# Optimization experiments

Hardware: AMD Instinct MI355X
Metric: run time of the kernel (lower is better)

Reference implementation:

```python
import jax, jax.numpy as jnp
import numpy as np

N = 50000      # nodes
E = 600000     # edges (avg degree 12)
D = 128        # input_dim == hidden_dim (required: same Linear reused across pool layers)
OUT = 64       # output_dim
NUM_POOL = 2   # num_pool_layers


def setup_inputs() -> dict:
    key = jax.random.key(0)
    ks = jax.random.split(key, 8)
    s = 1.0 / np.sqrt(D)  # fan-in style scaling keeps repeated scatter-adds stable
    x = jax.random.normal(ks[0], (N, D), dtype=jnp.float32)
    edge_index = jax.random.randint(ks[1], (2, E), 0, N, dtype=jnp.int64)
    W1 = jax.random.normal(ks[2], (D, D), dtype=jnp.float32) * s
    b1 = jnp.zeros((D,), dtype=jnp.float32)
    W2 = jax.random.normal(ks[3], (D, D), dtype=jnp.float32) * s
    b2 = jnp.zeros((D,), dtype=jnp.float32)
    Wout = jax.random.normal(ks[4], (D, OUT), dtype=jnp.float32) * s
    bout = jnp.zeros((OUT,), dtype=jnp.float32)
    return {"x": x, "edge_index": edge_index, "W1": W1, "b1": b1,
            "W2": W2, "b2": b2, "Wout": Wout, "bout": bout}


def _gauss_seidel_pool(x, W, b, src, dst, num_layers):
    # PyG MessagePassing(aggr='add'): out[i] = sum_{edges (j->i)} lin(x[j]).
    # Nodes with no incoming edges become zero (propagate replaces x entirely).
    for _ in range(num_layers):
        m = x @ W + b                      # [N, out] linear once per node (== lin(x_j) per edge)
        x = jax.ops.segment_sum(m[src], dst, num_segments=N)  # gather + scatter-add
    return x


def reference(x, edge_index, W1, b1, W2, b2, Wout, bout):
    src = edge_index[0]  # x_j source
    dst = edge_index[1]  # aggregation target i
    h = _gauss_seidel_pool(x, W1, b1, src, dst, NUM_POOL)
    h = jax.nn.relu(h)                     # dropout = identity (eval mode)
    h = _gauss_seidel_pool(h, W2, b2, src, dst, NUM_POOL)
    h = jax.nn.relu(h)
    return h @ Wout + bout                 # [N, OUT]
```

## Files before the change

kernel.cpp:

```cpp
#include <hip/hip_runtime.h>


static inline int ceil_div(int a, int b) { return (a + b - 1) / b; }

typedef __attribute__((ext_vector_type(8))) short bf16x8;
typedef __attribute__((ext_vector_type(4))) float f32x4;

__device__ inline unsigned short f2bf(float f) {
    unsigned u = __float_as_uint(f);
    return (unsigned short)((u + 0x7fffu + ((u >> 16) & 1u)) >> 16);
}


__device__ void wprep_dev(const float* __restrict__ W, unsigned short* __restrict__ hi,
                          int total, int C, int g0, int G) {
    for (int t = g0; t < total; t += G) {
        int j = t & 7;
        int lane = (t >> 3) & 63;
        int f = t >> 9;
        int c = f & 3, ct = f >> 2;
        int k = c * 32 + (lane >> 4) * 8 + j;
        int col = ct * 16 + (lane & 15);
        hi[t] = f2bf(W[(size_t)k * C + col]);
    }
}

__global__ __launch_bounds__(256) void prep_kernel(const float* __restrict__ x,
                                                   const float* __restrict__ W1,
                                                   const float* __restrict__ W2,
                                                   const float* __restrict__ Wout,
                                                   unsigned short* __restrict__ xb,
                                                   unsigned short* __restrict__ W1hi,
                                                   unsigned short* __restrict__ W2hi,
                                                   unsigned short* __restrict__ Wohi,
                                                   int* __restrict__ cursor,
                                                   unsigned* __restrict__ stat,
                                                   int N, int nChunks) {
    int g0 = blockIdx.x * 256 + threadIdx.x;
    int G = gridDim.x * 256;
    for (int i = g0; i < N; i += G) cursor[i] = 0;
    for (int i = g0; i < nChunks; i += G) stat[i] = 0;

    int nq = N * 32;
    for (int i = g0; i < nq; i += G) {
        float4 v = ((const float4*)x)[i];
        ushort4 o;
        o.x = f2bf(v.x); o.y = f2bf(v.y); o.z = f2bf(v.z); o.w = f2bf(v.w);
        ((ushort4*)xb)[i] = o;
    }

    wprep_dev(W1, W1hi, 128 * 128, 128, g0, G);
    wprep_dev(W2, W2hi, 128 * 128, 128, g0, G);
    wprep_dev(Wout, Wohi, 128 * 64, 64, g0, G);
}


__global__ __launch_bounds__(256) void hist_kernel(const int* __restrict__ dst,
                                                   int* __restrict__ deg, int E) {
    int e = blockIdx.x * 256 + threadIdx.x;
    if (e < E) atomicAdd(&deg[dst[e]], 1);
}

__global__ __launch_bounds__(256) void scan_fuse_kernel(const int* __restrict__ deg,
                                                        int* __restrict__ rp,
                                                        int* __restrict__ cursor,
                                                        unsigned* __restrict__ stat,
                                                        int N) {
    __shared__ int s[256];
    int c = blockIdx.x, tid = threadIdx.x;
    int i = c * 256 + tid;
    int v = (i < N) ? deg[i] : 0;
    s[tid] = v;
    __syncthreads();
    for (int off = 1; off < 256; off <<= 1) {
        int t = (tid >= off) ? s[tid - off] : 0;
        __syncthreads();
        s[tid] += t;
        __syncthreads();
    }
    int loc = s[tid] - v;
    int tot = s[255];
    __syncthreads();
    if (tid == 0) atomicExch(&stat[c], (unsigned)tot | 0x80000000u);

    unsigned mine = 0;
    if (tid < c) {
        unsigned u;
        do { u = atomicAdd(&stat[tid], 0u); } while (!(u & 0x80000000u));
        mine = u & 0x7fffffffu;
    }
    s[tid] = (int)mine;
    __syncthreads();
    for (int off = 128; off >= 1; off >>= 1) {
        if (tid < off) s[tid] += s[tid + off];
        __syncthreads();
    }
    int prefix = s[0];
    if (i <= N) {
        int val = loc + prefix;
        rp[i] = val;
        if (i < N) cursor[i] = val;
    }
}

__global__ __launch_bounds__(256) void fill_kernel(const int* __restrict__ src,
                                                   const int* __restrict__ dst,
                                                   int* __restrict__ cursor,
                                                   unsigned short* __restrict__ es, int E) {
    int e = blockIdx.x * 256 + threadIdx.x;
    if (e < E) {
        int p = atomicAdd(&cursor[dst[e]], 1);
        es[p] = (unsigned short)src[e];
    }
}


__device__ inline void acc_row8(float* a, uint4 v) {
    a[0] += __uint_as_float(v.x << 16);
    a[1] += __uint_as_float(v.x & 0xffff0000u);
    a[2] += __uint_as_float(v.y << 16);
    a[3] += __uint_as_float(v.y & 0xffff0000u);
    a[4] += __uint_as_float(v.z << 16);
    a[5] += __uint_as_float(v.z & 0xffff0000u);
    a[6] += __uint_as_float(v.w << 16);
    a[7] += __uint_as_float(v.w & 0xffff0000u);
}

template <bool RELU, bool OUTCHAIN>
__global__ __launch_bounds__(256) void fused_kernel(const unsigned short* __restrict__ M,
                                                    const int* __restrict__ rp,
                                                    const unsigned short* __restrict__ es,
                                                    const uint4* __restrict__ Whi,
                                                    const float* __restrict__ bvec,
                                                    const uint4* __restrict__ Wof,
                                                    const float* __restrict__ bout,
                                                    void* __restrict__ Yv, int n) {
    constexpr int SR = 136;
    __shared__ unsigned short Hl[64 * SR];
    __shared__ int rpl[65];
    __shared__ unsigned char perm[64];

    int tid = threadIdx.x;
    int r0 = blockIdx.x * 64;

    if (tid < 65) {
        int gi = r0 + tid;
        if (gi > n) gi = n;
        rpl[tid] = rp[gi];
    }
    __syncthreads();

    if (tid < 64) {
        int di = rpl[tid + 1] - rpl[tid];
        int rank = 0;
        for (int j = 0; j < 64; ++j) {
            int dj = rpl[j + 1] - rpl[j];
            rank += (dj > di) || (dj == di && j < tid);
        }
        perm[rank] = (unsigned char)tid;
    }
    __syncthreads();

    {
        int g = tid >> 4, ln = tid & 15;
#pragma unroll 1
        for (int q = 0; q < 4; ++q) {
            int nl = perm[q * 16 + g];
            int beg = rpl[nl], end = rpl[nl + 1];
            float acc[8] = {};
            int e = beg;
            for (; e + 8 <= end; e += 8) {
                int s0 = es[e],     s1 = es[e + 1], s2 = es[e + 2], s3 = es[e + 3];
                int s4 = es[e + 4], s5 = es[e + 5], s6 = es[e + 6], s7 = es[e + 7];
                uint4 v0 = ((const uint4*)(M + (size_t)s0 * 128))[ln];
                uint4 v1 = ((const uint4*)(M + (size_t)s1 * 128))[ln];
                uint4 v2 = ((const uint4*)(M + (size_t)s2 * 128))[ln];
                uint4 v3 = ((const uint4*)(M + (size_t)s3 * 128))[ln];
                uint4 v4 = ((const uint4*)(M + (size_t)s4 * 128))[ln];
                uint4 v5 = ((const uint4*)(M + (size_t)s5 * 128))[ln];
                uint4 v6 = ((const uint4*)(M + (size_t)s6 * 128))[ln];
                uint4 v7 = ((const uint4*)(M + (size_t)s7 * 128))[ln];
                acc_row8(acc, v0); acc_row8(acc, v1);
                acc_row8(acc, v2); acc_row8(acc, v3);
                acc_row8(acc, v4); acc_row8(acc, v5);
                acc_row8(acc, v6); acc_row8(acc, v7);
            }
            for (; e + 4 <= end; e += 4) {
                int s0 = es[e], s1 = es[e + 1], s2 = es[e + 2], s3 = es[e + 3];
                uint4 v0 = ((const uint4*)(M + (size_t)s0 * 128))[ln];
                uint4 v1 = ((const uint4*)(M + (size_t)s1 * 128))[ln];
                uint4 v2 = ((const uint4*)(M + (size_t)s2 * 128))[ln];
                uint4 v3 = ((const uint4*)(M + (size_t)s3 * 128))[ln];
                acc_row8(acc, v0); acc_row8(acc, v1);
                acc_row8(acc, v2); acc_row8(acc, v3);
            }
            for (; e < end; ++e) {
                uint4 v = ((const uint4*)(M + (size_t)es[e] * 128))[ln];
                acc_row8(acc, v);
            }
            uint4 o;
            o.x = (unsigned)f2bf(acc[0]) | ((unsigned)f2bf(acc[1]) << 16);
            o.y = (unsigned)f2bf(acc[2]) | ((unsigned)f2bf(acc[3]) << 16);
            o.z = (unsigned)f2bf(acc[4]) | ((unsigned)f2bf(acc[5]) << 16);
            o.w = (unsigned)f2bf(acc[6]) | ((unsigned)f2bf(acc[7]) << 16);
            *(uint4*)(&Hl[nl * SR + ln * 8]) = o;
        }
    }
    __syncthreads();

    int wave = tid >> 6, lane = tid & 63;
    int lm = lane & 15, lq = lane >> 4;

    f32x4 acc[4][2];
#pragma unroll
    for (int rt = 0; rt < 4; ++rt)
#pragma unroll
        for (int t = 0; t < 2; ++t)
            acc[rt][t] = (f32x4){0.f, 0.f, 0.f, 0.f};

#pragma unroll
    for (int c = 0; c < 4; ++c) {
        bf16x8 afr[4];
#pragma unroll
        for (int rt = 0; rt < 4; ++rt)
            afr[rt] = *(const bf16x8*)(&Hl[(rt * 16 + lm) * SR + c * 32 + lq * 8]);
#pragma unroll
        for (int t = 0; t < 2; ++t) {
            int ct = wave * 2 + t;
            uint4 uh = Whi[(ct * 4 + c) * 64 + lane];
            bf16x8 wh = *(const bf16x8*)&uh;
#pragma unroll
            for (int rt = 0; rt < 4; ++rt)
                acc[rt][t] = __builtin_amdgcn_mfma_f32_16x16x32_bf16(afr[rt], wh, acc[rt][t], 0, 0, 0);
        }
    }

    if (!OUTCHAIN) {
#pragma unroll
        for (int t = 0; t < 2; ++t) {
            int col = (wave * 2 + t) * 16 + lm;
            float bv = bvec[col];
#pragma unroll
            for (int rt = 0; rt < 4; ++rt) {
#pragma unroll
                for (int r = 0; r < 4; ++r) {
                    int rowl = rt * 16 + lq * 4 + r;
                    int row = r0 + rowl;
                    if (row < n) {
                        float deg = (float)(rpl[rowl + 1] - rpl[rowl]);
                        float v = acc[rt][t][r] + deg * bv;
                        if (RELU) v = fmaxf(v, 0.f);
                        ((unsigned short*)Yv)[(size_t)row * 128 + col] = f2bf(v);
                    }
                }
            }
        }
    } else {
        __syncthreads();
#pragma unroll
        for (int t = 0; t < 2; ++t) {
            int col = (wave * 2 + t) * 16 + lm;
            float bv = bvec[col];
#pragma unroll
            for (int rt = 0; rt < 4; ++rt) {
#pragma unroll
                for (int r = 0; r < 4; ++r) {
                    int rowl = rt * 16 + lq * 4 + r;
                    float deg = (float)(rpl[rowl + 1] - rpl[rowl]);
                    float v = acc[rt][t][r] + deg * bv;
                    v = fmaxf(v, 0.f);
                    Hl[rowl * SR + col] = f2bf(v);
                }
            }
        }
        __syncthreads();

        f32x4 acc2[4];
#pragma unroll
        for (int rt = 0; rt < 4; ++rt) acc2[rt] = (f32x4){0.f, 0.f, 0.f, 0.f};

#pragma unroll
        for (int c = 0; c < 4; ++c) {
            bf16x8 afr[4];
#pragma unroll
            for (int rt = 0; rt < 4; ++rt)
                afr[rt] = *(const bf16x8*)(&Hl[(rt * 16 + lm) * SR + c * 32 + lq * 8]);
            uint4 uw = Wof[(wave * 4 + c) * 64 + lane];
            bf16x8 wf = *(const bf16x8*)&uw;
#pragma unroll
            for (int rt = 0; rt < 4; ++rt)
                acc2[rt] = __builtin_amdgcn_mfma_f32_16x16x32_bf16(afr[rt], wf, acc2[rt], 0, 0, 0);
        }

        int col = wave * 16 + lm;
        float bo = bout[col];
#pragma unroll
        for (int rt = 0; rt < 4; ++rt) {
#pragma unroll
            for (int r = 0; r < 4; ++r) {
                int row = r0 + rt * 16 + lq * 4 + r;
                if (row < n)
                    ((float*)Yv)[(size_t)row * 64 + col] = acc2[rt][r] + bo;
            }
        }
    }
}


extern "C" void kernel_launch(void* const* d_in, const int* in_sizes, int n_in,
                              void* d_out, int out_size, void* d_ws, size_t ws_size,
                              hipStream_t stream) {
    const float* x    = (const float*)d_in[0];
    const int*   ei   = (const int*)d_in[1];
    const float* W1   = (const float*)d_in[2];
    const float* b1   = (const float*)d_in[3];
    const float* W2   = (const float*)d_in[4];
    const float* b2   = (const float*)d_in[5];
    const float* Wout = (const float*)d_in[6];
    const float* bout = (const float*)d_in[7];
    float*       out  = (float*)d_out;

    const int N = in_sizes[0] / 128;
    const int E = in_sizes[1] / 2;
    const int* src = ei;
    const int* dst = ei + E;

    char* ws = (char*)d_ws;
    auto take = [&](size_t bytes) {
        char* p = ws;
        ws += (bytes + 255) & ~(size_t)255;
        return p;
    };
    unsigned short* xb = (unsigned short*)take((size_t)N * 128 * 2);
    unsigned short* mA = (unsigned short*)take((size_t)N * 128 * 2);
    unsigned short* mB = (unsigned short*)take((size_t)N * 128 * 2);
    unsigned short* W1hi = (unsigned short*)take(128 * 128 * 2);
    unsigned short* W2hi = (unsigned short*)take(128 * 128 * 2);
    unsigned short* Wohi = (unsigned short*)take(128 * 64 * 2);
    int* rp      = (int*)take((size_t)(N + 1) * sizeof(int));
    int* cursor  = (int*)take((size_t)N * sizeof(int));
    unsigned short* es = (unsigned short*)take((size_t)E * sizeof(unsigned short));
    unsigned* stat = (unsigned*)take(4096);

    const int nChunks = ceil_div(N + 1, 256);
    const int tiles64 = ceil_div(N, 64);

    prep_kernel<<<256, 256, 0, stream>>>(x, W1, W2, Wout, xb, W1hi, W2hi, Wohi,
                                         cursor, stat, N, nChunks);
    hist_kernel<<<ceil_div(E, 256), 256, 0, stream>>>(dst, cursor, E);
    scan_fuse_kernel<<<nChunks, 256, 0, stream>>>(cursor, rp, cursor, stat, N);
    fill_kernel<<<ceil_div(E, 256), 256, 0, stream>>>(src, dst, cursor, es, E);

    fused_kernel<false, false><<<tiles64, 256, 0, stream>>>(
        xb, rp, es, (const uint4*)W1hi, b1, nullptr, nullptr, mA, N);
    fused_kernel<true, false><<<tiles64, 256, 0, stream>>>(
        mA, rp, es, (const uint4*)W1hi, b1, nullptr, nullptr, mB, N);
    fused_kernel<false, false><<<tiles64, 256, 0, stream>>>(
        mB, rp, es, (const uint4*)W2hi, b2, nullptr, nullptr, mA, N);
    fused_kernel<true, true><<<tiles64, 256, 0, stream>>>(
        mA, rp, es, (const uint4*)W2hi, b2, (const uint4*)Wohi, bout, out, N);
}
```

Before: 275.6 us.

## Use 512-thread blocks with degree-balanced gather pairing and per-wave MFMA column tiles

```diff
diff --git a/kernel.cpp b/kernel.cpp
--- a/kernel.cpp
+++ b/kernel.cpp
@@ -127,7 +127,7 @@
 }
 
 template <bool RELU, bool OUTCHAIN>
-__global__ __launch_bounds__(256) void fused_kernel(const unsigned short* __restrict__ M,
+__global__ __launch_bounds__(512) void fused_kernel(const unsigned short* __restrict__ M,
                                                     const int* __restrict__ rp,
                                                     const unsigned short* __restrict__ es,
                                                     const uint4* __restrict__ Whi,
@@ -164,8 +164,8 @@
     {
         int g = tid >> 4, ln = tid & 15;
 #pragma unroll 1
-        for (int q = 0; q < 4; ++q) {
-            int nl = perm[q * 16 + g];
+        for (int q = 0; q < 2; ++q) {
+            int nl = perm[q ? (63 - g) : g];
             int beg = rpl[nl], end = rpl[nl + 1];
             float acc[8] = {};
             int e = beg;
@@ -211,12 +211,10 @@
     int wave = tid >> 6, lane = tid & 63;
     int lm = lane & 15, lq = lane >> 4;
 
-    f32x4 acc[4][2];
+    f32x4 acc[4];
 #pragma unroll
     for (int rt = 0; rt < 4; ++rt)
-#pragma unroll
-        for (int t = 0; t < 2; ++t)
-            acc[rt][t] = (f32x4){0.f, 0.f, 0.f, 0.f};
+        acc[rt] = (f32x4){0.f, 0.f, 0.f, 0.f};
 
 #pragma unroll
     for (int c = 0; c < 4; ++c) {
@@ -224,42 +222,34 @@
 #pragma unroll
         for (int rt = 0; rt < 4; ++rt)
             afr[rt] = *(const bf16x8*)(&Hl[(rt * 16 + lm) * SR + c * 32 + lq * 8]);
-#pragma unroll
-        for (int t = 0; t < 2; ++t) {
-            int ct = wave * 2 + t;
-            uint4 uh = Whi[(ct * 4 + c) * 64 + lane];
-            bf16x8 wh = *(const bf16x8*)&uh;
-#pragma unroll
-            for (int rt = 0; rt < 4; ++rt)
-                acc[rt][t] = __builtin_amdgcn_mfma_f32_16x16x32_bf16(afr[rt], wh, acc[rt][t], 0, 0, 0);
-        }
+        uint4 uh = Whi[(wave * 4 + c) * 64 + lane];
+        bf16x8 wh = *(const bf16x8*)&uh;
+#pragma unroll
+        for (int rt = 0; rt < 4; ++rt)
+            acc[rt] = __builtin_amdgcn_mfma_f32_16x16x32_bf16(afr[rt], wh, acc[rt], 0, 0, 0);
     }
 
     if (!OUTCHAIN) {
-#pragma unroll
-        for (int t = 0; t < 2; ++t) {
-            int col = (wave * 2 + t) * 16 + lm;
-            float bv = bvec[col];
-#pragma unroll
-            for (int rt = 0; rt < 4; ++rt) {
-#pragma unroll
-                for (int r = 0; r < 4; ++r) {
-                    int rowl = rt * 16 + lq * 4 + r;
-                    int row = r0 + rowl;
-                    if (row < n) {
-                        float deg = (float)(rpl[rowl + 1] - rpl[rowl]);
-                        float v = acc[rt][t][r] + deg * bv;
-                        if (RELU) v = fmaxf(v, 0.f);
-                        ((unsigned short*)Yv)[(size_t)row * 128 + col] = f2bf(v);
-                    }
+        int col = wave * 16 + lm;
+        float bv = bvec[col];
+#pragma unroll
+        for (int rt = 0; rt < 4; ++rt) {
+#pragma unroll
+            for (int r = 0; r < 4; ++r) {
+                int rowl = rt * 16 + lq * 4 + r;
+                int row = r0 + rowl;
+                if (row < n) {
+                    float deg = (float)(rpl[rowl + 1] - rpl[rowl]);
+                    float v = acc[rt][r] + deg * bv;
+                    if (RELU) v = fmaxf(v, 0.f);
+                    ((unsigned short*)Yv)[(size_t)row * 128 + col] = f2bf(v);
                 }
             }
         }
     } else {
         __syncthreads();
-#pragma unroll
-        for (int t = 0; t < 2; ++t) {
-            int col = (wave * 2 + t) * 16 + lm;
+        {
+            int col = wave * 16 + lm;
             float bv = bvec[col];
 #pragma unroll
             for (int rt = 0; rt < 4; ++rt) {
@@ -267,7 +257,7 @@
                 for (int r = 0; r < 4; ++r) {
                     int rowl = rt * 16 + lq * 4 + r;
                     float deg = (float)(rpl[rowl + 1] - rpl[rowl]);
-                    float v = acc[rt][t][r] + deg * bv;
+                    float v = acc[rt][r] + deg * bv;
                     v = fmaxf(v, 0.f);
                     Hl[rowl * SR + col] = f2bf(v);
                 }
@@ -275,32 +265,32 @@
         }
         __syncthreads();
 
-        f32x4 acc2[4];
-#pragma unroll
-        for (int rt = 0; rt < 4; ++rt) acc2[rt] = (f32x4){0.f, 0.f, 0.f, 0.f};
+        int prt = wave >> 1;
+        int ctb = (wave & 1) * 2;
+        f32x4 acc2[2];
+#pragma unroll
+        for (int i = 0; i < 2; ++i) acc2[i] = (f32x4){0.f, 0.f, 0.f, 0.f};
 
 #pragma unroll
         for (int c = 0; c < 4; ++c) {
-            bf16x8 afr[4];
-#pragma unroll
-            for (int rt = 0; rt < 4; ++rt)
-                afr[rt] = *(const bf16x8*)(&Hl[(rt * 16 + lm) * SR + c * 32 + lq * 8]);
-            uint4 uw = Wof[(wave * 4 + c) * 64 + lane];
-            bf16x8 wf = *(const bf16x8*)&uw;
-#pragma unroll
-            for (int rt = 0; rt < 4; ++rt)
-                acc2[rt] = __builtin_amdgcn_mfma_f32_16x16x32_bf16(afr[rt], wf, acc2[rt], 0, 0, 0);
-        }
-
-        int col = wave * 16 + lm;
-        float bo = bout[col];
-#pragma unroll
-        for (int rt = 0; rt < 4; ++rt) {
+            bf16x8 afr = *(const bf16x8*)(&Hl[(prt * 16 + lm) * SR + c * 32 + lq * 8]);
+#pragma unroll
+            for (int i = 0; i < 2; ++i) {
+                uint4 uw = Wof[((ctb + i) * 4 + c) * 64 + lane];
+                bf16x8 wf = *(const bf16x8*)&uw;
+                acc2[i] = __builtin_amdgcn_mfma_f32_16x16x32_bf16(afr, wf, acc2[i], 0, 0, 0);
+            }
+        }
+
+#pragma unroll
+        for (int i = 0; i < 2; ++i) {
+            int col = (ctb + i) * 16 + lm;
+            float bo = bout[col];
 #pragma unroll
             for (int r = 0; r < 4; ++r) {
-                int row = r0 + rt * 16 + lq * 4 + r;
+                int row = r0 + prt * 16 + lq * 4 + r;
                 if (row < n)
-                    ((float*)Yv)[(size_t)row * 64 + col] = acc2[rt][r] + bo;
+                    ((float*)Yv)[(size_t)row * 64 + col] = acc2[i][r] + bo;
             }
         }
     }
@@ -351,12 +341,12 @@
     scan_fuse_kernel<<<nChunks, 256, 0, stream>>>(cursor, rp, cursor, stat, N);
     fill_kernel<<<ceil_div(E, 256), 256, 0, stream>>>(src, dst, cursor, es, E);
 
-    fused_kernel<false, false><<<tiles64, 256, 0, stream>>>(
+    fused_kernel<false, false><<<tiles64, 512, 0, stream>>>(
         xb, rp, es, (const uint4*)W1hi, b1, nullptr, nullptr, mA, N);
-    fused_kernel<true, false><<<tiles64, 256, 0, stream>>>(
+    fused_kernel<true, false><<<tiles64, 512, 0, stream>>>(
         mA, rp, es, (const uint4*)W1hi, b1, nullptr, nullptr, mB, N);
-    fused_kernel<false, false><<<tiles64, 256, 0, stream>>>(
+    fused_kernel<false, false><<<tiles64, 512, 0, stream>>>(
         mB, rp, es, (const uint4*)W2hi, b2, nullptr, nullptr, mA, N);
-    fused_kernel<true, true><<<tiles64, 256, 0, stream>>>(
+    fused_kernel<true, true><<<tiles64, 512, 0, stream>>>(
         mA, rp, es, (const uint4*)W2hi, b2, (const uint4*)Wohi, bout, out, N);
 }
```

New measurement: 292.5 us. 6.1% more time.
